# Kernel optimization log

Measured on AMD Instinct MI355X. Metric: run time of the kernel, lower is better.

Reference implementation:

```python
import jax, jax.numpy as jnp
from jax import lax
import numpy as np

G = 32        # voxel grid resolution per axis (pres=vres=1 -> voxel = floor(coord))
N = 100000    # number of points
C = 96        # hidden_dim == input_dim


def _voxelize(feats, coords):
    """initial_voxelize: average point features per voxel. Returns (grid (G^3,C), occ (G^3,) bool, flat idx)."""
    vox = jnp.clip(jnp.floor(coords).astype(jnp.int32), 0, G - 1)
    flat = (vox[:, 0] * G + vox[:, 1]) * G + vox[:, 2]
    sums = jax.ops.segment_sum(feats, flat, num_segments=G ** 3)
    cnt = jax.ops.segment_sum(jnp.ones((feats.shape[0],), feats.dtype), flat, num_segments=G ** 3)
    grid = sums / jnp.maximum(cnt, 1.0)[:, None]
    return grid, cnt > 0


def _sconv(feats, coords, conv_w, lin_w, lin_b):
    """SConv3d: voxelize -> submanifold 3x3x3 conv (outputs only at occupied voxels)
    -> trilinear devoxelize (missing voxels contribute 0) -> + Linear(feats)."""
    Cin = feats.shape[1]
    Cout = conv_w.shape[0]
    grid, occ = _voxelize(feats, coords)
    g = grid.reshape(G, G, G, Cin).transpose(3, 0, 1, 2)[None]          # (1,Cin,G,G,G)
    out = lax.conv_general_dilated(g, conv_w, (1, 1, 1), 'SAME',
                                   dimension_numbers=('NCDHW', 'OIDHW', 'NCDHW'))
    out = out * occ.reshape(1, 1, G, G, G)                               # submanifold: keep input coords only
    outv = out[0].transpose(1, 2, 3, 0).reshape(G ** 3, Cout)            # (G^3,Cout)
    base = jnp.floor(coords)
    f = coords - base                                                    # trilinear fractions (N,3)
    basei = base.astype(jnp.int32)
    devox = jnp.zeros((feats.shape[0], Cout), feats.dtype)
    for dx in (0, 1):
        for dy in (0, 1):
            for dz in (0, 1):
                c = basei + jnp.array([dx, dy, dz], jnp.int32)
                valid = jnp.all((c >= 0) & (c < G), axis=1)
                cc = jnp.clip(c, 0, G - 1)
                flc = (cc[:, 0] * G + cc[:, 1]) * G + cc[:, 2]
                w = ((f[:, 0] if dx else 1.0 - f[:, 0]) *
                     (f[:, 1] if dy else 1.0 - f[:, 1]) *
                     (f[:, 2] if dz else 1.0 - f[:, 2]))
                w = w * (valid & occ[flc]).astype(w.dtype)
                devox = devox + outv[flc] * w[:, None]
    return devox + feats @ lin_w.T + lin_b


def setup_inputs() -> dict:
    key = jax.random.key(0)
    ks = jax.random.split(key, 20)
    def conv(k, o, i):
        return jax.random.normal(k, (o, i, 3, 3, 3), jnp.float32) / np.sqrt(i * 27)
    def lin(k, o, i):
        k1, k2 = jax.random.split(k)
        return (jax.random.normal(k1, (o, i), jnp.float32) / np.sqrt(i),
                jax.random.normal(k2, (o,), jnp.float32) * 0.01)
    wq_lw, wq_lb = lin(ks[3], C, C)
    wh_lw, wh_lb = lin(ks[4], C, C)
    att_lw, att_lb = lin(ks[5], C, 2 * C)
    v_lw, v_lb = lin(ks[6], 1, C)
    upd_lw, upd_lb = lin(ks[7], C, 2 * C)
    return {
        'hidden': jax.random.normal(ks[0], (N, C), jnp.float32),
        'query': jax.random.normal(ks[1], (N, C), jnp.float32),
        'coords': jax.random.uniform(ks[2], (N, 3), jnp.float32) * G,
        'wq_conv': conv(ks[8], C, C), 'wq_lw': wq_lw, 'wq_lb': wq_lb,
        'wh_conv': conv(ks[9], C, C), 'wh_lw': wh_lw, 'wh_lb': wh_lb,
        'att_conv': conv(ks[10], C, 2 * C), 'att_lw': att_lw, 'att_lb': att_lb,
        'v_conv': conv(ks[11], 1, C), 'v_lw': v_lw, 'v_lb': v_lb,
        'upd_conv': conv(ks[12], C, 2 * C), 'upd_lw': upd_lw, 'upd_lb': upd_lb,
    }


def reference(hidden, query, coords,
              wq_conv, wq_lw, wq_lb,
              wh_conv, wh_lw, wh_lb,
              att_conv, att_lw, att_lb,
              v_conv, v_lw, v_lb,
              upd_conv, upd_lw, upd_lb):
    q = _sconv(query, coords, wq_conv, wq_lw, wq_lb)           # (N,C)
    h = _sconv(hidden, coords, wh_conv, wh_lw, wh_lb)          # (N,C)
    hx = jnp.concatenate([h, q], axis=1)                        # (N,2C)
    energy = jnp.tanh(_sconv(hx, coords, att_conv, att_lw, att_lb))
    attn = _sconv(energy, coords, v_conv, v_lw, v_lb)           # (N,1)
    context = attn * h                                          # attention-gated hidden
    qcat = jnp.concatenate([q, context], axis=1)                # (N,2C)
    return jnp.tanh(_sconv(qcat, coords, upd_conv, upd_lw, upd_lb))
```

## Files before the change

kernel.cpp:

```cpp
#include <hip/hip_runtime.h>
#include <math.h>


#define GD 32
#define NV (GD*GD*GD)
#define CH 96

typedef _Float16 half8 __attribute__((ext_vector_type(8)));
typedef _Float16 half4 __attribute__((ext_vector_type(4)));
typedef float f32x4 __attribute__((ext_vector_type(4)));


__global__ void k_prep(const float* __restrict__ coords, int* __restrict__ flat,
                       unsigned* __restrict__ cnt, int n) {
  int i = blockIdx.x * 256 + threadIdx.x;
  if (i >= n) return;
  float x = coords[3*i], y = coords[3*i+1], z = coords[3*i+2];
  int ix = (int)floorf(x); ix = ix < 0 ? 0 : (ix > 31 ? 31 : ix);
  int iy = (int)floorf(y); iy = iy < 0 ? 0 : (iy > 31 ? 31 : iy);
  int iz = (int)floorf(z); iz = iz < 0 ? 0 : (iz > 31 ? 31 : iz);
  int f = (ix << 10) + (iy << 5) + iz;
  flat[i] = f;
  atomicAdd(&cnt[f], 1u);
}

__global__ __launch_bounds__(1024) void k_scan(
    const unsigned* __restrict__ cnt, unsigned* __restrict__ base,
    unsigned* __restrict__ cur, float* __restrict__ inv) {
  __shared__ unsigned part[1024];
  int tid = threadIdx.x;
  int b0 = tid * 32;
  unsigned s = 0;
  for (int i = 0; i < 32; ++i) s += cnt[b0 + i];
  part[tid] = s;
  __syncthreads();
  for (int off = 1; off < 1024; off <<= 1) {
    unsigned t = (tid >= off) ? part[tid - off] : 0u;
    __syncthreads();
    if (tid >= off) part[tid] += t;
    __syncthreads();
  }
  unsigned run = part[tid] - s;
  for (int i = 0; i < 32; ++i) {
    int v = b0 + i;
    unsigned c = cnt[v];
    base[v] = run; cur[v] = run;
    inv[v] = c ? 1.0f / (float)c : 0.0f;
    run += c;
  }
}

__global__ void k_fill(const int* __restrict__ flat, unsigned* __restrict__ cur,
                       int* __restrict__ order, int n) {
  int p = blockIdx.x * 256 + threadIdx.x;
  if (p >= n) return;
  unsigned pos = atomicAdd(&cur[flat[p]], 1u);
  order[pos] = p;
}

template<int SCALED, int PAIR, int SRCF16>
__global__ void k_voxavg(const void* __restrict__ src, const float* __restrict__ scale,
                         const unsigned* __restrict__ base, const unsigned* __restrict__ cnt,
                         const float* __restrict__ inv, const int* __restrict__ order,
                         void* __restrict__ dst,
                         const void* __restrict__ src2, void* __restrict__ dst2) {
  int e = blockIdx.x * 256 + threadIdx.x;
  const void* sp = src; void* d = dst;
  if (PAIR && e >= NV * 24) { e -= NV * 24; sp = src2; d = dst2; }
  int v = e / 24, c4 = e - v * 24;
  unsigned b = base[v], c = cnt[v];
  f32x4 s = {0.f, 0.f, 0.f, 0.f};
  for (unsigned i = 0; i < c; ++i) {
    int p = order[b + i];
    f32x4 x;
    if (SRCF16) {
      half4 hx = __builtin_nontemporal_load(reinterpret_cast<const half4*>(sp) + p * 24 + c4);
      x = (f32x4){(float)hx[0], (float)hx[1], (float)hx[2], (float)hx[3]};
    } else {
      x = __builtin_nontemporal_load(reinterpret_cast<const f32x4*>(sp) + p * 24 + c4);
    }
    if (SCALED) x *= scale[p];
    s += x;
  }
  s *= inv[v];
  union { _Float16 h; unsigned short u; } h0, h1, h2, h3;
  h0.h = (_Float16)s.x; h1.h = (_Float16)s.y; h2.h = (_Float16)s.z; h3.h = (_Float16)s.w;
  ushort4 o; o.x = h0.u; o.y = h1.u; o.z = h2.u; o.w = h3.u;
  reinterpret_cast<ushort4*>(d)[e] = o;
}


__device__ __forceinline__ void wpack_one(int e, const float* __restrict__ w,
                                          _Float16* __restrict__ wp, int nch) {
  int j = e & 7; int l = (e >> 3) & 63; int r = e >> 9;
  int cot = r % 6; r /= 6; int chk = r % nch; int tap = r / nch;
  int Ci = nch * 32;
  int ci = chk * 32 + (l >> 4) * 8 + j;
  int co = cot * 16 + (l & 15);
  wp[e] = (_Float16)w[(co * Ci + ci) * 27 + tap];
}

__device__ __forceinline__ void linpack_one(int e, const float* __restrict__ w,
                                            _Float16* __restrict__ wl, int kb) {
  int j = e & 7; int l = (e >> 3) & 63; int r = e >> 9;
  int nt = r % 6; int kt = r / 6;
  int Ci = kb * 32;
  int ci = kt * 32 + (l >> 4) * 8 + j;
  int co = nt * 16 + (l & 15);
  wl[e] = (_Float16)w[co * Ci + ci];
}

#define WP3 (27*3*6*512)
#define WP6 (27*6*6*512)
#define WL3 (3*6*512)
#define WL6 (6*6*512)
#define WV2 (27*512)
#define PACK_TOTAL (2*WP3 + 2*WP6 + 2*WL3 + 2*WL6 + WV2)

__global__ void k_packall(
    const float* __restrict__ wq, const float* __restrict__ wh,
    const float* __restrict__ wa, const float* __restrict__ wu,
    const float* __restrict__ lq, const float* __restrict__ lh,
    const float* __restrict__ la, const float* __restrict__ lu,
    const float* __restrict__ wvc,
    _Float16* __restrict__ wpq, _Float16* __restrict__ wph,
    _Float16* __restrict__ wpa, _Float16* __restrict__ wpu,
    _Float16* __restrict__ wlq, _Float16* __restrict__ wlh,
    _Float16* __restrict__ wla, _Float16* __restrict__ wlu,
    _Float16* __restrict__ wt2) {
  int e = blockIdx.x * 256 + threadIdx.x;
  if (e < WP3) { wpack_one(e, wq, wpq, 3); return; } e -= WP3;
  if (e < WP3) { wpack_one(e, wh, wph, 3); return; } e -= WP3;
  if (e < WP6) { wpack_one(e, wa, wpa, 6); return; } e -= WP6;
  if (e < WP6) { wpack_one(e, wu, wpu, 6); return; } e -= WP6;
  if (e < WL3) { linpack_one(e, lq, wlq, 3); return; } e -= WL3;
  if (e < WL3) { linpack_one(e, lh, wlh, 3); return; } e -= WL3;
  if (e < WL6) { linpack_one(e, la, wla, 6); return; } e -= WL6;
  if (e < WL6) { linpack_one(e, lu, wlu, 6); return; } e -= WL6;
  if (e < WV2) {
    int j = e & 7; int l = (e >> 3) & 63; int r = e >> 9;
    int col9 = r % 9, chunk = r / 9;
    int n = l & 15, kq = l >> 4;
    int ci = chunk * 32 + kq * 8 + j;
    wt2[e] = (n < 3) ? (_Float16)wvc[ci * 27 + col9 * 3 + n] : (_Float16)0.f;
  }
}

template<int NCH, int PAIR>
__global__ __launch_bounds__(384, 4) void k_conv_mfma(
    const _Float16* __restrict__ gA, const _Float16* __restrict__ gB,
    const half8* __restrict__ wp, _Float16* __restrict__ out,
    const _Float16* __restrict__ gA2, const half8* __restrict__ wp2,
    _Float16* __restrict__ out2) {
  __shared__ unsigned short ls[12 * 34 * 40];
  int bid = blockIdx.x;
  const _Float16* ga = gA; const _Float16* gb = gB;
  const half8* w = wp; _Float16* o = out;
  if (PAIR && bid >= 512) { bid -= 512; ga = gA2; gb = gA2; w = wp2; o = out2; }
  int bx = bid >> 4, y0 = (bid & 15) * 2;
  int tid = threadIdx.x;
  int lane = tid & 63, wv = tid >> 6;
  int msel = wv & 1, npair = wv >> 1;
  int lrow = lane & 15, quad = lane >> 4;

  f32x4 acc[2][2];
#pragma unroll
  for (int i = 0; i < 2; ++i)
#pragma unroll
    for (int j = 0; j < 2; ++j) acc[i][j] = (f32x4){0.f, 0.f, 0.f, 0.f};

  for (int chunk = 0; chunk < NCH; ++chunk) {
    const _Float16* g = (NCH == 6 && chunk >= 3) ? gb : ga;
    int cbase = ((NCH == 6 && chunk >= 3) ? chunk - 3 : chunk) * 32;
    __syncthreads();
    for (int e = tid; e < 12 * 34 * 4; e += 384) {
      int ciu = e & 3; int zc = e >> 2;
      int zz = zc % 34; int sc = zc / 34;
      int dx = sc >> 2, dyy = sc & 3;
      int x = bx + dx - 1, y = y0 + dyy - 1, zv = zz - 1;
      uint4 val = {0u, 0u, 0u, 0u};
      if ((unsigned)x < 32u && (unsigned)y < 32u && (unsigned)zv < 32u)
        val = *reinterpret_cast<const uint4*>(
            g + (size_t)((x << 10) + (y << 5) + zv) * CH + cbase + ciu * 8);
      *reinterpret_cast<uint4*>(&ls[(sc * 34 + zz) * 40 + ciu * 8]) = val;
    }
    __syncthreads();
#pragma unroll
    for (int dx9 = 0; dx9 < 3; ++dx9)
#pragma unroll
      for (int dy9 = 0; dy9 < 3; ++dy9) {
        int sc = dx9 * 4 + msel + dy9;
        const unsigned short* lbase = &ls[(sc * 34) * 40 + quad * 8];
        int tap0 = (dx9 * 3 + dy9) * 3;
#pragma unroll
        for (int dz = 0; dz < 3; ++dz) {
          half8 a0 = *reinterpret_cast<const half8*>(&lbase[(lrow + dz) * 40]);
          half8 a1 = *reinterpret_cast<const half8*>(&lbase[(16 + lrow + dz) * 40]);
          const half8* wb = w + ((size_t)((tap0 + dz) * NCH + chunk) * 6 + npair * 2) * 64 + lane;
          half8 b0 = wb[0];
          half8 b1 = wb[64];
          acc[0][0] = __builtin_amdgcn_mfma_f32_16x16x32_f16(a0, b0, acc[0][0], 0, 0, 0);
          acc[1][0] = __builtin_amdgcn_mfma_f32_16x16x32_f16(a1, b0, acc[1][0], 0, 0, 0);
          acc[0][1] = __builtin_amdgcn_mfma_f32_16x16x32_f16(a0, b1, acc[0][1], 0, 0, 0);
          acc[1][1] = __builtin_amdgcn_mfma_f32_16x16x32_f16(a1, b1, acc[1][1], 0, 0, 0);
        }
      }
  }
  int y = y0 + msel;
  int vb = (bx << 10) + (y << 5);
#pragma unroll
  for (int mt = 0; mt < 2; ++mt)
#pragma unroll
    for (int nb = 0; nb < 2; ++nb)
#pragma unroll
      for (int r = 0; r < 4; ++r) {
        int z = mt * 16 + quad * 4 + r;
        o[(size_t)(vb + z) * CH + (npair * 2 + nb) * 16 + lrow] = (_Float16)acc[mt][nb][r];
      }
}

__global__ __launch_bounds__(128) void k_conv3d_v2(
    const _Float16* __restrict__ g, const _Float16* __restrict__ wt2,
    float* __restrict__ out) {
  __shared__ unsigned short ls[12 * 48 * 32];
  __shared__ float dl[2][48][4];
  int bid = blockIdx.x;
  int bx = bid >> 4, y0 = (bid & 15) * 2;
  int tid = threadIdx.x;
  int lane = tid & 63, wv = tid >> 6;
  int lrow = lane & 15, quad = lane >> 4;

  f32x4 acc[3];
#pragma unroll
  for (int i = 0; i < 3; ++i) acc[i] = (f32x4){0.f, 0.f, 0.f, 0.f};

  for (int chunk = 0; chunk < 3; ++chunk) {
    __syncthreads();
#pragma unroll 3
    for (int it = 0; it < 18; ++it) {
      int e = it * 128 + tid;
      int c8 = e & 3;
      int t = e >> 2;
      int col = t / 48;
      int zz = t - col * 48;
      int dx = col >> 2, dyy = col & 3;
      int x = bx + dx - 1, y = y0 + dyy - 1, zv = zz - 1;
      uint4 val = {0u, 0u, 0u, 0u};
      if ((unsigned)x < 32u && (unsigned)y < 32u && (unsigned)zv < 32u)
        val = *reinterpret_cast<const uint4*>(
            g + (size_t)((x << 10) + (y << 5) + zv) * CH + chunk * 32 + c8 * 8);
      *reinterpret_cast<uint4*>(&ls[(t << 5) + ((c8 ^ (zz & 3)) << 3)]) = val;
    }
    __syncthreads();
#pragma unroll
    for (int dx9 = 0; dx9 < 3; ++dx9)
#pragma unroll
      for (int dy9 = 0; dy9 < 3; ++dy9) {
        int col9 = dx9 * 3 + dy9;
        int sc = dx9 * 4 + wv + dy9;
        half8 b = *reinterpret_cast<const half8*>(
            wt2 + (size_t)((chunk * 9 + col9) << 9) + (lane << 3));
#pragma unroll
        for (int mt = 0; mt < 3; ++mt) {
          int zz = mt * 16 + lrow;
          half8 a = *reinterpret_cast<const half8*>(
              &ls[((sc * 48 + zz) << 5) + ((quad ^ (zz & 3)) << 3)]);
          acc[mt] = __builtin_amdgcn_mfma_f32_16x16x32_f16(a, b, acc[mt], 0, 0, 0);
        }
      }
  }
  if (lrow < 3) {
#pragma unroll
    for (int mt = 0; mt < 3; ++mt)
#pragma unroll
      for (int r = 0; r < 4; ++r)
        dl[wv][mt * 16 + quad * 4 + r][lrow] = acc[mt][r];
  }
  __syncthreads();
  if (tid < 64) {
    int z = tid & 31, yb = tid >> 5;
    float v = dl[yb][z][0] + dl[yb][z + 1][1] + dl[yb][z + 2][2];
    out[(bx << 10) + ((y0 + yb) << 5) + z] = v;
  }
}


__device__ __forceinline__ void corner_one(
    const float* __restrict__ coords, const unsigned* __restrict__ cnt,
    int p, int k, int& flc, float& w) {
  float cx = coords[3*p], cy = coords[3*p+1], cz = coords[3*p+2];
  float bx = floorf(cx), by = floorf(cy), bz = floorf(cz);
  float fx = cx - bx, fy = cy - by, fz = cz - bz;
  int dx = (k >> 2) & 1, dy = (k >> 1) & 1, dzz = k & 1;
  int ix = (int)bx + dx, iy = (int)by + dy, iz = (int)bz + dzz;
  bool valid = ((unsigned)ix < 32u) && ((unsigned)iy < 32u) && ((unsigned)iz < 32u);
  int xc = min(max(ix, 0), 31), yc = min(max(iy, 0), 31), zc = min(max(iz, 0), 31);
  flc = (xc << 10) + (yc << 5) + zc;
  float wx = dx ? fx : 1.f - fx;
  float wy = dy ? fy : 1.f - fy;
  float wz = dzz ? fz : 1.f - fz;
  w = (valid && cnt[flc] > 0u) ? wx * wy * wz : 0.f;
}

template<int KB, int MODE, int PAIR>
__global__ __launch_bounds__(256) void k_point(
    const _Float16* __restrict__ outv, const void* __restrict__ X1, const void* __restrict__ X2,
    const float* __restrict__ scale, const half8* __restrict__ wl,
    const float* __restrict__ lb, const float* __restrict__ vlw,
    const float* __restrict__ coords, const unsigned* __restrict__ cnt,
    void* __restrict__ dst, float* __restrict__ attn_out, int n,
    const _Float16* __restrict__ outv2, const void* __restrict__ X1b,
    const half8* __restrict__ wl2, const float* __restrict__ lb2,
    void* __restrict__ dst2) {
  __shared__ char us[64 * 100 * 4];
  __shared__ int lflc[512];
  __shared__ float lcw[512];
  constexpr int APITCH = KB * 32 + 8;
  constexpr int XF16 = (KB == 6);
  constexpr int OUTF16 = (MODE != 2);
  int tid = threadIdx.x;
  int bid = blockIdx.x;
  const _Float16* ov = outv; const void* x1 = X1;
  const half8* w = wl; const float* b = lb; void* d = dst;
  if (PAIR) {
    int npt = (n + 63) >> 6;
    if (bid >= npt) { bid -= npt; ov = outv2; x1 = X1b; w = wl2; b = lb2; d = dst2; }
  }
  int p0 = bid * 64;

  for (int e = tid; e < 512; e += 256) {
    int j = e >> 3, k = e & 7, p = p0 + j;
    int f = 0; float wgt = 0.f;
    if (p < n) corner_one(coords, cnt, p, k, f, wgt);
    lflc[e] = f; lcw[e] = wgt;
  }

  unsigned short* lsa = reinterpret_cast<unsigned short*>(us);
  constexpr int T4 = 64 * KB * 8;
  for (int e = tid; e < T4; e += 256) {
    int j = e / (KB * 8);
    int q4 = e - j * (KB * 8);
    int p = p0 + j;
    if (XF16) {
      half4 hx = {(_Float16)0.f, (_Float16)0.f, (_Float16)0.f, (_Float16)0.f};
      if (p < n) {
        if (q4 < 24) {
          hx = __builtin_nontemporal_load(reinterpret_cast<const half4*>(x1) + p * 24 + q4);
        } else {
          hx = __builtin_nontemporal_load(reinterpret_cast<const half4*>(X2) + p * 24 + (q4 - 24));
          if (MODE == 2) {
            float sc = scale[p];
            hx = (half4){(_Float16)((float)hx[0] * sc), (_Float16)((float)hx[1] * sc),
                         (_Float16)((float)hx[2] * sc), (_Float16)((float)hx[3] * sc)};
          }
        }
      }
      *reinterpret_cast<half4*>(&lsa[j * APITCH + q4 * 4]) = hx;
    } else {
      f32x4 v = {0.f, 0.f, 0.f, 0.f};
      if (p < n)
        v = __builtin_nontemporal_load(reinterpret_cast<const f32x4*>(x1) + p * 24 + q4);
      union { _Float16 h; unsigned short u; } h0, h1, h2, h3;
      h0.h = (_Float16)v.x; h1.h = (_Float16)v.y; h2.h = (_Float16)v.z; h3.h = (_Float16)v.w;
      ushort4 o; o.x = h0.u; o.y = h1.u; o.z = h2.u; o.w = h3.u;
      *reinterpret_cast<ushort4*>(&lsa[j * APITCH + q4 * 4]) = o;
    }
  }
  __syncthreads();

  int lane = tid & 63, wv = tid >> 6;
  int lrow = lane & 15, quad = lane >> 4;
  f32x4 acc[6];
#pragma unroll
  for (int i = 0; i < 6; ++i) acc[i] = (f32x4){0.f, 0.f, 0.f, 0.f};
#pragma unroll
  for (int kt = 0; kt < KB; ++kt) {
    half8 a = *reinterpret_cast<const half8*>(&lsa[(wv * 16 + lrow) * APITCH + kt * 32 + quad * 8]);
    const half8* wb = w + (size_t)(kt * 6) * 64 + lane;
#pragma unroll
    for (int nt = 0; nt < 6; ++nt)
      acc[nt] = __builtin_amdgcn_mfma_f32_16x16x32_f16(a, wb[(size_t)nt * 64], acc[nt], 0, 0, 0);
  }
  __syncthreads();
  float* lacc = reinterpret_cast<float*>(us);
#pragma unroll
  for (int nt = 0; nt < 6; ++nt)
#pragma unroll
    for (int r = 0; r < 4; ++r)
      lacc[(wv * 16 + quad * 4 + r) * 100 + nt * 16 + lrow] = acc[nt][r];
  __syncthreads();

  int pt = tid >> 2, sub = tid & 3;
  int p = p0 + pt;
  f32x4 a[6];
  const float* lrow_p = &lacc[pt * 100 + sub * 24];
#pragma unroll
  for (int i = 0; i < 6; ++i) a[i] = *reinterpret_cast<const f32x4*>(lrow_p + i * 4);
  const f32x4* lb4 = reinterpret_cast<const f32x4*>(b + sub * 24);
#pragma unroll
  for (int i = 0; i < 6; ++i) a[i] += lb4[i];
#pragma unroll
  for (int k = 0; k < 8; ++k) {
    float wgt = lcw[pt * 8 + k];
    if (wgt != 0.f) {
      const half8* op = reinterpret_cast<const half8*>(ov + (size_t)lflc[pt * 8 + k] * CH + sub * 24);
      half8 o0 = op[0], o1 = op[1], o2 = op[2];
      f32x4 t;
      t = (f32x4){(float)o0[0], (float)o0[1], (float)o0[2], (float)o0[3]}; a[0] += wgt * t;
      t = (f32x4){(float)o0[4], (float)o0[5], (float)o0[6], (float)o0[7]}; a[1] += wgt * t;
      t = (f32x4){(float)o1[0], (float)o1[1], (float)o1[2], (float)o1[3]}; a[2] += wgt * t;
      t = (f32x4){(float)o1[4], (float)o1[5], (float)o1[6], (float)o1[7]}; a[3] += wgt * t;
      t = (f32x4){(float)o2[0], (float)o2[1], (float)o2[2], (float)o2[3]}; a[4] += wgt * t;
      t = (f32x4){(float)o2[4], (float)o2[5], (float)o2[6], (float)o2[7]}; a[5] += wgt * t;
    }
  }
  if (MODE >= 1) {
#pragma unroll
    for (int i = 0; i < 6; ++i) {
      a[i].x = tanhf(a[i].x); a[i].y = tanhf(a[i].y);
      a[i].z = tanhf(a[i].z); a[i].w = tanhf(a[i].w);
    }
  }
  if (p < n) {
    if (OUTF16) {
      _Float16* dh = reinterpret_cast<_Float16*>(d) + (size_t)p * CH + sub * 24;
      uint4* du = reinterpret_cast<uint4*>(dh);
#pragma unroll
      for (int i = 0; i < 3; ++i) {
        union { _Float16 h[8]; uint4 q; } t;
        t.h[0] = (_Float16)a[2*i].x;   t.h[1] = (_Float16)a[2*i].y;
        t.h[2] = (_Float16)a[2*i].z;   t.h[3] = (_Float16)a[2*i].w;
        t.h[4] = (_Float16)a[2*i+1].x; t.h[5] = (_Float16)a[2*i+1].y;
        t.h[6] = (_Float16)a[2*i+1].z; t.h[7] = (_Float16)a[2*i+1].w;
        du[i] = t.q;
      }
    } else {
      f32x4* d4 = reinterpret_cast<f32x4*>(d) + (size_t)p * 24 + sub * 6;
#pragma unroll
      for (int i = 0; i < 6; ++i) d4[i] = a[i];
    }
  }
  if (MODE == 1) {
    const f32x4* vw4 = reinterpret_cast<const f32x4*>(vlw + sub * 24);
    float partial = 0.f;
#pragma unroll
    for (int i = 0; i < 6; ++i) {
      f32x4 vw = vw4[i];
      partial += a[i].x * vw.x + a[i].y * vw.y + a[i].z * vw.z + a[i].w * vw.w;
    }
    partial += __shfl_xor(partial, 1);
    partial += __shfl_xor(partial, 2);
    if (sub == 0 && p < n) attn_out[p] = partial;
  }
}

__global__ void k_attn_final(const float* __restrict__ outvV, const float* __restrict__ vlb,
                             const float* __restrict__ coords, const unsigned* __restrict__ cnt,
                             float* __restrict__ attn, int n) {
  int p = blockIdx.x * 256 + threadIdx.x;
  if (p >= n) return;
  float a = attn[p] + vlb[0];
#pragma unroll
  for (int k = 0; k < 8; ++k) {
    int f; float w;
    corner_one(coords, cnt, p, k, f, w);
    a += w * outvV[f];
  }
  attn[p] = a;
}


extern "C" void kernel_launch(void* const* d_in, const int* in_sizes, int n_in,
                              void* d_out, int out_size, void* d_ws, size_t ws_size,
                              hipStream_t stream) {
  const float* hidden   = (const float*)d_in[0];
  const float* query    = (const float*)d_in[1];
  const float* coords   = (const float*)d_in[2];
  const float* wq_conv  = (const float*)d_in[3];
  const float* wq_lw    = (const float*)d_in[4];
  const float* wq_lb    = (const float*)d_in[5];
  const float* wh_conv  = (const float*)d_in[6];
  const float* wh_lw    = (const float*)d_in[7];
  const float* wh_lb    = (const float*)d_in[8];
  const float* att_conv = (const float*)d_in[9];
  const float* att_lw   = (const float*)d_in[10];
  const float* att_lb   = (const float*)d_in[11];
  const float* v_conv   = (const float*)d_in[12];
  const float* v_lw     = (const float*)d_in[13];
  const float* v_lb     = (const float*)d_in[14];
  const float* upd_conv = (const float*)d_in[15];
  const float* upd_lw   = (const float*)d_in[16];
  const float* upd_lb   = (const float*)d_in[17];
  float* out = (float*)d_out;
  const int n = in_sizes[0] / CH;

  char* wsp = (char*)d_ws;
  auto alloc = [&](size_t bytes) {
    char* r = wsp;
    wsp += (bytes + 255) & ~(size_t)255;
    return r;
  };
  int*      flat  = (int*)     alloc((size_t)n * 4);
  int*      order = (int*)     alloc((size_t)n * 4);
  unsigned* cnt   = (unsigned*)alloc((size_t)NV * 4);
  unsigned* base  = (unsigned*)alloc((size_t)NV * 4);
  unsigned* cur   = (unsigned*)alloc((size_t)NV * 4);
  float*    inv   = (float*)   alloc((size_t)NV * 4);
  float*    attn  = (float*)   alloc((size_t)n * 4);
  _Float16* wt2   = (_Float16*)alloc((size_t)WV2 * 2);
  _Float16* wpq = (_Float16*)alloc((size_t)WP3 * 2);
  _Float16* wph = (_Float16*)alloc((size_t)WP3 * 2);
  _Float16* wpa = (_Float16*)alloc((size_t)WP6 * 2);
  _Float16* wpu = (_Float16*)alloc((size_t)WP6 * 2);
  _Float16* wlq = (_Float16*)alloc((size_t)WL3 * 2);
  _Float16* wlh = (_Float16*)alloc((size_t)WL3 * 2);
  _Float16* wla = (_Float16*)alloc((size_t)WL6 * 2);
  _Float16* wlu = (_Float16*)alloc((size_t)WL6 * 2);
  _Float16* Hq  = (_Float16*)alloc((size_t)NV * CH * 2);
  _Float16* Hh  = (_Float16*)alloc((size_t)NV * CH * 2);
  _Float16* H1  = (_Float16*)alloc((size_t)NV * CH * 2);
  _Float16* H2  = (_Float16*)alloc((size_t)NV * CH * 2);
  _Float16* O1  = (_Float16*)alloc((size_t)NV * CH * 2);
  _Float16* O2  = (_Float16*)alloc((size_t)NV * CH * 2);
  float* Ov   = (float*)alloc((size_t)NV * 4);
  _Float16* qv   = (_Float16*)alloc((size_t)n * CH * 2);
  _Float16* hv   = (_Float16*)alloc((size_t)n * CH * 2);
  _Float16* ebuf = (_Float16*)alloc((size_t)n * CH * 2);

  const int nb  = (n + 255) / 256;
  const int npt = (n + 63) / 64;
  const int nva = NV * 24 / 256;

  hipMemsetAsync(cnt, 0, (size_t)NV * 4, stream);
  k_prep<<<nb, 256, 0, stream>>>(coords, flat, cnt, n);
  k_scan<<<1, 1024, 0, stream>>>(cnt, base, cur, inv);
  k_fill<<<nb, 256, 0, stream>>>(flat, cur, order, n);
  k_packall<<<(PACK_TOTAL + 255) / 256, 256, 0, stream>>>(
      wq_conv, wh_conv, att_conv, upd_conv, wq_lw, wh_lw, att_lw, upd_lw, v_conv,
      wpq, wph, wpa, wpu, wlq, wlh, wla, wlu, wt2);

  k_voxavg<0,1,0><<<2*nva, 256, 0, stream>>>(query, nullptr, base, cnt, inv, order,
                                             Hq, hidden, Hh);
  k_conv_mfma<3,1><<<1024, 384, 0, stream>>>(Hq, Hq, (const half8*)wpq, O1,
                                             Hh, (const half8*)wph, O2);
  k_point<3,0,1><<<2*npt, 256, 0, stream>>>(O1, query, nullptr, nullptr, (const half8*)wlq,
                                            wq_lb, nullptr, coords, cnt, qv, nullptr, n,
                                            O2, hidden, (const half8*)wlh, wh_lb, hv);

  k_voxavg<0,1,1><<<2*nva, 256, 0, stream>>>(hv, nullptr, base, cnt, inv, order,
                                             H1, qv, H2);
  k_conv_mfma<6,0><<<512, 384, 0, stream>>>(H1, H2, (const half8*)wpa, O1,
                                            nullptr, nullptr, nullptr);
  k_point<6,1,0><<<npt, 256, 0, stream>>>(O1, hv, qv, nullptr, (const half8*)wla,
                                          att_lb, v_lw, coords, cnt, ebuf, attn, n,
                                          nullptr, nullptr, nullptr, nullptr, nullptr);

  k_voxavg<0,0,1><<<nva, 256, 0, stream>>>(ebuf, nullptr, base, cnt, inv, order,
                                           Hq, nullptr, nullptr);
  k_conv3d_v2<<<512, 128, 0, stream>>>(Hq, wt2, Ov);
  k_attn_final<<<nb, 256, 0, stream>>>(Ov, v_lb, coords, cnt, attn, n);

  k_voxavg<1,0,1><<<nva, 256, 0, stream>>>(hv, attn, base, cnt, inv, order,
                                           H1, nullptr, nullptr);
  k_conv_mfma<6,0><<<512, 384, 0, stream>>>(H2, H1, (const half8*)wpu, O1,
                                            nullptr, nullptr, nullptr);
  k_point<6,2,0><<<npt, 256, 0, stream>>>(O1, qv, hv, attn, (const half8*)wlu,
                                          upd_lb, nullptr, coords, cnt, out, nullptr, n,
                                          nullptr, nullptr, nullptr, nullptr, nullptr);
}
```

Measured before the change: 639.1 us.

## Keep intermediate point buffers in voxel-sorted order to make voxel averaging contiguous

```diff
diff --git a/kernel.cpp b/kernel.cpp
--- a/kernel.cpp
+++ b/kernel.cpp
@@ -58,7 +58,7 @@
   order[pos] = p;
 }
 
-template<int SCALED, int PAIR, int SRCF16>
+template<int SCALED, int PAIR, int SRCF16, int SORTED>
 __global__ void k_voxavg(const void* __restrict__ src, const float* __restrict__ scale,
                          const unsigned* __restrict__ base, const unsigned* __restrict__ cnt,
                          const float* __restrict__ inv, const int* __restrict__ order,
@@ -71,7 +71,7 @@
   unsigned b = base[v], c = cnt[v];
   f32x4 s = {0.f, 0.f, 0.f, 0.f};
   for (unsigned i = 0; i < c; ++i) {
-    int p = order[b + i];
+    int p = SORTED ? (int)(b + i) : order[b + i];
     f32x4 x;
     if (SRCF16) {
       half4 hx = __builtin_nontemporal_load(reinterpret_cast<const half4*>(sp) + p * 24 + c4);
@@ -308,6 +308,7 @@
     const float* __restrict__ scale, const half8* __restrict__ wl,
     const float* __restrict__ lb, const float* __restrict__ vlw,
     const float* __restrict__ coords, const unsigned* __restrict__ cnt,
+    const int* __restrict__ order,
     void* __restrict__ dst, float* __restrict__ attn_out, int n,
     const _Float16* __restrict__ outv2, const void* __restrict__ X1b,
     const half8* __restrict__ wl2, const float* __restrict__ lb2,
@@ -315,6 +316,7 @@
   __shared__ char us[64 * 100 * 4];
   __shared__ int lflc[512];
   __shared__ float lcw[512];
+  __shared__ int lord[64];
   constexpr int APITCH = KB * 32 + 8;
   constexpr int XF16 = (KB == 6);
   constexpr int OUTF16 = (MODE != 2);
@@ -328,10 +330,13 @@
   }
   int p0 = bid * 64;
 
+  if (tid < 64) lord[tid] = (p0 + tid < n) ? order[p0 + tid] : 0;
+  __syncthreads();
+
   for (int e = tid; e < 512; e += 256) {
-    int j = e >> 3, k = e & 7, p = p0 + j;
+    int j = e >> 3, k = e & 7;
     int f = 0; float wgt = 0.f;
-    if (p < n) corner_one(coords, cnt, p, k, f, wgt);
+    if (p0 + j < n) corner_one(coords, cnt, lord[j], k, f, wgt);
     lflc[e] = f; lcw[e] = wgt;
   }
 
@@ -340,16 +345,16 @@
   for (int e = tid; e < T4; e += 256) {
     int j = e / (KB * 8);
     int q4 = e - j * (KB * 8);
-    int p = p0 + j;
+    int idx = p0 + j;
     if (XF16) {
       half4 hx = {(_Float16)0.f, (_Float16)0.f, (_Float16)0.f, (_Float16)0.f};
-      if (p < n) {
+      if (idx < n) {
         if (q4 < 24) {
-          hx = __builtin_nontemporal_load(reinterpret_cast<const half4*>(x1) + p * 24 + q4);
+          hx = __builtin_nontemporal_load(reinterpret_cast<const half4*>(x1) + idx * 24 + q4);
         } else {
-          hx = __builtin_nontemporal_load(reinterpret_cast<const half4*>(X2) + p * 24 + (q4 - 24));
+          hx = __builtin_nontemporal_load(reinterpret_cast<const half4*>(X2) + idx * 24 + (q4 - 24));
           if (MODE == 2) {
-            float sc = scale[p];
+            float sc = scale[idx];
             hx = (half4){(_Float16)((float)hx[0] * sc), (_Float16)((float)hx[1] * sc),
                          (_Float16)((float)hx[2] * sc), (_Float16)((float)hx[3] * sc)};
           }
@@ -358,8 +363,9 @@
       *reinterpret_cast<half4*>(&lsa[j * APITCH + q4 * 4]) = hx;
     } else {
       f32x4 v = {0.f, 0.f, 0.f, 0.f};
-      if (p < n)
-        v = __builtin_nontemporal_load(reinterpret_cast<const f32x4*>(x1) + p * 24 + q4);
+      if (idx < n)
+        v = __builtin_nontemporal_load(
+            reinterpret_cast<const f32x4*>(x1) + (size_t)lord[j] * 24 + q4);
       union { _Float16 h; unsigned short u; } h0, h1, h2, h3;
       h0.h = (_Float16)v.x; h1.h = (_Float16)v.y; h2.h = (_Float16)v.z; h3.h = (_Float16)v.w;
       ushort4 o; o.x = h0.u; o.y = h1.u; o.z = h2.u; o.w = h3.u;
@@ -391,7 +397,8 @@
   __syncthreads();
 
   int pt = tid >> 2, sub = tid & 3;
-  int p = p0 + pt;
+  int idx = p0 + pt;
+  bool valid = idx < n;
   f32x4 a[6];
   const float* lrow_p = &lacc[pt * 100 + sub * 24];
 #pragma unroll
@@ -421,9 +428,9 @@
       a[i].z = tanhf(a[i].z); a[i].w = tanhf(a[i].w);
     }
   }
-  if (p < n) {
+  if (valid) {
     if (OUTF16) {
-      _Float16* dh = reinterpret_cast<_Float16*>(d) + (size_t)p * CH + sub * 24;
+      _Float16* dh = reinterpret_cast<_Float16*>(d) + (size_t)idx * CH + sub * 24;
       uint4* du = reinterpret_cast<uint4*>(dh);
 #pragma unroll
       for (int i = 0; i < 3; ++i) {
@@ -435,7 +442,7 @@
         du[i] = t.q;
       }
     } else {
-      f32x4* d4 = reinterpret_cast<f32x4*>(d) + (size_t)p * 24 + sub * 6;
+      f32x4* d4 = reinterpret_cast<f32x4*>(d) + (size_t)lord[pt] * 24 + sub * 6;
 #pragma unroll
       for (int i = 0; i < 6; ++i) d4[i] = a[i];
     }
@@ -450,23 +457,25 @@
     }
     partial += __shfl_xor(partial, 1);
     partial += __shfl_xor(partial, 2);
-    if (sub == 0 && p < n) attn_out[p] = partial;
+    if (sub == 0 && valid) attn_out[idx] = partial;
   }
 }
 
 __global__ void k_attn_final(const float* __restrict__ outvV, const float* __restrict__ vlb,
                              const float* __restrict__ coords, const unsigned* __restrict__ cnt,
+                             const int* __restrict__ order,
                              float* __restrict__ attn, int n) {
-  int p = blockIdx.x * 256 + threadIdx.x;
-  if (p >= n) return;
-  float a = attn[p] + vlb[0];
+  int idx = blockIdx.x * 256 + threadIdx.x;
+  if (idx >= n) return;
+  int p = order[idx];
+  float a = attn[idx] + vlb[0];
 #pragma unroll
   for (int k = 0; k < 8; ++k) {
     int f; float w;
     corner_one(coords, cnt, p, k, f, w);
     a += w * outvV[f];
   }
-  attn[p] = a;
+  attn[idx] = a;
 }
 
 
@@ -539,32 +548,32 @@
       wq_conv, wh_conv, att_conv, upd_conv, wq_lw, wh_lw, att_lw, upd_lw, v_conv,
       wpq, wph, wpa, wpu, wlq, wlh, wla, wlu, wt2);
 
-  k_voxavg<0,1,0><<<2*nva, 256, 0, stream>>>(query, nullptr, base, cnt, inv, order,
-                                             Hq, hidden, Hh);
+  k_voxavg<0,1,0,0><<<2*nva, 256, 0, stream>>>(query, nullptr, base, cnt, inv, order,
+                                               Hq, hidden, Hh);
   k_conv_mfma<3,1><<<1024, 384, 0, stream>>>(Hq, Hq, (const half8*)wpq, O1,
                                              Hh, (const half8*)wph, O2);
   k_point<3,0,1><<<2*npt, 256, 0, stream>>>(O1, query, nullptr, nullptr, (const half8*)wlq,
-                                            wq_lb, nullptr, coords, cnt, qv, nullptr, n,
+                                            wq_lb, nullptr, coords, cnt, order, qv, nullptr, n,
                                             O2, hidden, (const half8*)wlh, wh_lb, hv);
 
-  k_voxavg<0,1,1><<<2*nva, 256, 0, stream>>>(hv, nullptr, base, cnt, inv, order,
-                                             H1, qv, H2);
+  k_voxavg<0,1,1,1><<<2*nva, 256, 0, stream>>>(hv, nullptr, base, cnt, inv, order,
+                                               H1, qv, H2);
   k_conv_mfma<6,0><<<512, 384, 0, stream>>>(H1, H2, (const half8*)wpa, O1,
                                             nullptr, nullptr, nullptr);
   k_point<6,1,0><<<npt, 256, 0, stream>>>(O1, hv, qv, nullptr, (const half8*)wla,
-                                          att_lb, v_lw, coords, cnt, ebuf, attn, n,
+                                          att_lb, v_lw, coords, cnt, order, ebuf, attn, n,
                                           nullptr, nullptr, nullptr, nullptr, nullptr);
 
-  k_voxavg<0,0,1><<<nva, 256, 0, stream>>>(ebuf, nullptr, base, cnt, inv, order,
-                                           Hq, nullptr, nullptr);
+  k_voxavg<0,0,1,1><<<nva, 256, 0, stream>>>(ebuf, nullptr, base, cnt, inv, order,
+                                             Hq, nullptr, nullptr);
   k_conv3d_v2<<<512, 128, 0, stream>>>(Hq, wt2, Ov);
-  k_attn_final<<<nb, 256, 0, stream>>>(Ov, v_lb, coords, cnt, attn, n);
-
-  k_voxavg<1,0,1><<<nva, 256, 0, stream>>>(hv, attn, base, cnt, inv, order,
-                                           H1, nullptr, nullptr);
+  k_attn_final<<<nb, 256, 0, stream>>>(Ov, v_lb, coords, cnt, order, attn, n);
+
+  k_voxavg<1,0,1,1><<<nva, 256, 0, stream>>>(hv, attn, base, cnt, inv, order,
+                                             H1, nullptr, nullptr);
   k_conv_mfma<6,0><<<512, 384, 0, stream>>>(H2, H1, (const half8*)wpu, O1,
                                             nullptr, nullptr, nullptr);
   k_point<6,2,0><<<npt, 256, 0, stream>>>(O1, qv, hv, attn, (const half8*)wlu,
-                                          upd_lb, nullptr, coords, cnt, out, nullptr, n,
+                                          upd_lb, nullptr, coords, cnt, order, out, nullptr, n,
                                           nullptr, nullptr, nullptr, nullptr, nullptr);
 }
```

Result: faster. 604.4 us (-5.4%).
